# Kernel tuning notes

Measured on AMD Instinct MI355X. Metric: run time of the kernel, lower is better.

The kernel has to match this reference:

```python
import jax, jax.numpy as jnp
import numpy as np

N = 50000       # nodes
E = 800000      # edges
D_IN = 128      # input_dim
HID = 256       # hidden_dim
HEADS = 4
FH = HID // 4   # per-head out dim = 64
OUT = 8         # output_dim
NEG_SLOPE = 0.2 # GATConv leaky_relu slope


def setup_inputs() -> dict:
    key = jax.random.key(0)
    ks = jax.random.split(key, 16)
    def glorot(k, shape):
        fan_in, fan_out = shape[0], shape[-1]
        s = jnp.sqrt(6.0 / (fan_in + fan_out))
        return jax.random.uniform(k, shape, jnp.float32, -s, s)
    inp = {
        "x": jax.random.normal(ks[0], (N, D_IN), jnp.float32),
        "edge_index": jax.random.randint(ks[1], (2, E), 0, N, jnp.int64),
        # GCN layers
        "W1": glorot(ks[2], (D_IN, HID)), "b1": jnp.zeros((HID,), jnp.float32),
        "W2": glorot(ks[3], (HID, HID)), "b2": jnp.zeros((HID,), jnp.float32),
        "W3": glorot(ks[4], (HID, HID // 2)), "b3": jnp.zeros((HID // 2,), jnp.float32),
        # GAT layer: in = HID//2 = 128, out per head = FH, 4 heads concat -> HID
        "Wg": glorot(ks[5], (HID // 2, HEADS * FH)),
        "a_src": glorot(ks[6], (HEADS, FH)),
        "a_dst": glorot(ks[7], (HEADS, FH)),
        "bg": jnp.zeros((HEADS * FH,), jnp.float32),
        # classifier MLP: HID -> HID//2 -> HID//4 -> OUT
        "Wc1": glorot(ks[8], (HID, HID // 2)), "bc1": jnp.zeros((HID // 2,), jnp.float32),
        "Wc2": glorot(ks[9], (HID // 2, HID // 4)), "bc2": jnp.zeros((HID // 4,), jnp.float32),
        "Wc3": glorot(ks[10], (HID // 4, OUT)), "bc3": jnp.zeros((OUT,), jnp.float32),
    }
    return inp


def _with_self_loops(edge_index, n):
    loop = jnp.arange(n, dtype=edge_index.dtype)
    src = jnp.concatenate([edge_index[0], loop])
    dst = jnp.concatenate([edge_index[1], loop])
    return src, dst


def gcn_conv(x, W, b, src, dst, n):
    # PyG GCNConv: h = X W; out = D^{-1/2}(A+I)D^{-1/2} h + b (self loops in src/dst)
    h = x @ W
    deg = jax.ops.segment_sum(jnp.ones_like(dst, jnp.float32), dst, num_segments=n)
    dinv = jnp.where(deg > 0, jax.lax.rsqrt(deg), 0.0)
    norm = dinv[src] * dinv[dst]                      # [E+N]
    out = jax.ops.segment_sum(h[src] * norm[:, None], dst, num_segments=n)
    return out + b


def gat_conv(x, Wg, a_src, a_dst, bg, src, dst, n):
    # PyG GATConv (eval mode, no attn dropout), self loops included in src/dst
    h = (x @ Wg).reshape(n, HEADS, FH)                # [N,H,F]
    al_s = jnp.einsum('nhf,hf->nh', h, a_src)         # [N,H]
    al_d = jnp.einsum('nhf,hf->nh', h, a_dst)
    e = jax.nn.leaky_relu(al_s[src] + al_d[dst], NEG_SLOPE)  # [E+N,H]
    m = jax.ops.segment_max(e, dst, num_segments=n)   # per-dst stable softmax
    ex = jnp.exp(e - m[dst])
    den = jax.ops.segment_sum(ex, dst, num_segments=n)
    alpha = ex / den[dst]                             # [E+N,H]
    out = jax.ops.segment_sum(h[src] * alpha[:, :, None], dst, num_segments=n)
    return out.reshape(n, HEADS * FH) + bg


def reference(x, edge_index, W1, b1, W2, b2, W3, b3, Wg, a_src, a_dst, bg,
              Wc1, bc1, Wc2, bc2, Wc3, bc3):
    n = x.shape[0]
    src, dst = _with_self_loops(edge_index, n)
    h1 = jax.nn.relu(gcn_conv(x, W1, b1, src, dst, n))
    h2 = jax.nn.relu(gcn_conv(h1, W2, b2, src, dst, n)) + h1
    h3 = jax.nn.relu(gcn_conv(h2, W3, b3, src, dst, n))
    h_att = jax.nn.relu(gat_conv(h3, Wg, a_src, a_dst, bg, src, dst, n))
    h_pooled = jnp.mean(h_att, axis=0, keepdims=True)           # [1, HID]
    z = jax.nn.relu(h_pooled @ Wc1 + bc1)
    z = jax.nn.relu(z @ Wc2 + bc2)
    return z @ Wc3 + bc3                                        # [1, OUT]
```

## Files before the change

### kernel.cpp

```cpp
#include <hip/hip_runtime.h>
#include <hip/hip_bf16.h>

#define NNODES 50000
#define NEDGES 800000
#define EN 850000
#define SCAN_B 196

typedef __attribute__((ext_vector_type(8))) short bf16x8;
typedef __attribute__((ext_vector_type(4))) float f32x4;

__device__ __forceinline__ float bf2f(unsigned short u) {
    return __uint_as_float(((unsigned)u) << 16);
}
__device__ __forceinline__ float bflo(unsigned u) { return __uint_as_float(u << 16); }
__device__ __forceinline__ float bfhi(unsigned u) { return __uint_as_float(u & 0xffff0000u); }
__device__ __forceinline__ unsigned short f2bf(float x) {
    unsigned u = __float_as_uint(x);
    u += 0x7fffu + ((u >> 16) & 1u);
    return (unsigned short)(u >> 16);
}
__device__ __forceinline__ unsigned pack2bf(float a, float b) {
    return (unsigned)f2bf(a) | ((unsigned)f2bf(b) << 16);
}
__device__ __forceinline__ void acc8(float* acc, uint4 v, float wg) {
    acc[0] += bflo(v.x) * wg; acc[1] += bfhi(v.x) * wg;
    acc[2] += bflo(v.y) * wg; acc[3] += bfhi(v.y) * wg;
    acc[4] += bflo(v.z) * wg; acc[5] += bfhi(v.z) * wg;
    acc[6] += bflo(v.w) * wg; acc[7] += bfhi(v.w) * wg;
}

__global__ __launch_bounds__(256) void deg_kernel(const int* __restrict__ ei, float* __restrict__ deg) {
    int e = blockIdx.x * blockDim.x + threadIdx.x;
    if (e < NEDGES) atomicAdd(&deg[ei[NEDGES + e]], 1.0f);
}

__global__ __launch_bounds__(256) void scan_part1(const float* __restrict__ deg, int* __restrict__ row,
                                                  int* __restrict__ bsum, float* __restrict__ dinv) {
    __shared__ int sdata[256];
    int t = threadIdx.x;
    int idx = blockIdx.x * 256 + t;
    float dg = idx < NNODES ? deg[idx] : 0.f;
    if (idx < NNODES) dinv[idx] = rsqrtf(dg + 1.0f);
    int v = idx < NNODES ? (int)dg + 1 : 0;
    sdata[t] = v;
    __syncthreads();
    for (int off = 1; off < 256; off <<= 1) {
        int tmp = t >= off ? sdata[t - off] : 0;
        __syncthreads();
        sdata[t] += tmp;
        __syncthreads();
    }
    if (idx < NNODES) row[idx] = sdata[t] - v;
    if (t == 255) bsum[blockIdx.x] = sdata[255];
}

__global__ __launch_bounds__(256) void scan_part2(int* __restrict__ bsum, int* __restrict__ bofs,
                                                  int* __restrict__ row) {
    __shared__ int sdata[256];
    int t = threadIdx.x;
    int v = t < SCAN_B ? bsum[t] : 0;
    sdata[t] = v;
    __syncthreads();
    for (int off = 1; off < 256; off <<= 1) {
        int tmp = t >= off ? sdata[t - off] : 0;
        __syncthreads();
        sdata[t] += tmp;
        __syncthreads();
    }
    if (t < SCAN_B) bofs[t] = sdata[t] - v;
    if (t == 0) row[NNODES] = EN;
}

__global__ __launch_bounds__(256) void scan_part3(int* __restrict__ row, const int* __restrict__ bofs) {
    int idx = blockIdx.x * 256 + threadIdx.x;
    if (idx < NNODES) row[idx] += bofs[blockIdx.x];
}

__global__ __launch_bounds__(256) void scatter_kernel(const int* __restrict__ ei, const int* __restrict__ row,
                                                      int* __restrict__ cursor, const float* __restrict__ dinv,
                                                      uint2* __restrict__ csr) {
    int e = blockIdx.x * blockDim.x + threadIdx.x;
    if (e >= EN) return;
    int s, d;
    if (e < NEDGES) { s = ei[e]; d = ei[NEDGES + e]; } else { s = e - NEDGES; d = s; }
    int pos = row[d] + atomicAdd(&cursor[d], 1);
    csr[pos] = make_uint2((unsigned)s, __float_as_uint(dinv[s] * dinv[d]));
}

__global__ __launch_bounds__(256) void tobf16_kernel(const float* __restrict__ in, unsigned short* __restrict__ out,
                                                     int total8) {
    int i = blockIdx.x * 256 + threadIdx.x;
    if (i >= total8) return;
    float4 a = *(const float4*)&in[(size_t)i * 8];
    float4 b = *(const float4*)&in[(size_t)i * 8 + 4];
    uint4 o;
    o.x = pack2bf(a.x, a.y); o.y = pack2bf(a.z, a.w);
    o.z = pack2bf(b.x, b.y); o.w = pack2bf(b.z, b.w);
    *(uint4*)&out[(size_t)i * 8] = o;
}

__device__ __forceinline__ void split_bf(float x, unsigned short& h, unsigned short& l) {
    unsigned u = __float_as_uint(x);
    h = (unsigned short)(u >> 16);
    float r = x - __uint_as_float(u & 0xffff0000u);
    l = (unsigned short)(__float_as_uint(r) >> 16);
}

__device__ __forceinline__ void do_split(const float* W, unsigned short* Wh, unsigned short* Wl,
                                         int i, int K, int N) {
    int n = i / K, k = i - n * K;
    unsigned short h, l;
    split_bf(W[(size_t)k * N + n], h, l);
    Wh[i] = h; Wl[i] = l;
}

__global__ __launch_bounds__(256) void wsplit4_kernel(const float* __restrict__ W1, const float* __restrict__ W2,
                                                      const float* __restrict__ W3, const float* __restrict__ Wg,
                                                      unsigned short* __restrict__ W1th, unsigned short* __restrict__ W1tl,
                                                      unsigned short* __restrict__ W2th, unsigned short* __restrict__ W2tl,
                                                      unsigned short* __restrict__ W3th, unsigned short* __restrict__ W3tl,
                                                      unsigned short* __restrict__ Wgth, unsigned short* __restrict__ Wgtl) {
    int idx = blockIdx.x * 256 + threadIdx.x;
    if (idx < 32768)        do_split(W1, W1th, W1tl, idx, 128, 256);
    else if (idx < 98304)   do_split(W2, W2th, W2tl, idx - 32768, 256, 256);
    else if (idx < 131072)  do_split(W3, W3th, W3tl, idx - 98304, 256, 128);
    else if (idx < 163840)  do_split(Wg, Wgth, Wgtl, idx - 131072, 128, 256);
}

template<int MODE>
__global__ __launch_bounds__(256) void gemm_bf(const unsigned short* __restrict__ A,
                                               const unsigned short* __restrict__ Wth,
                                               const unsigned short* __restrict__ Wtl,
                                               const float* __restrict__ bias,
                                               unsigned short* __restrict__ C, int M, int K, int Nc) {
    __shared__ unsigned short As[128][40];
    __shared__ unsigned short Bh[128][40], Bl[128][40];
    int t = threadIdx.x;
    int row0 = blockIdx.x * 128, col0 = blockIdx.y * 128;
    int lane = t & 63, w = t >> 6;
    int mb = (w >> 1) * 64, nb = (w & 1) * 64;
    int lr = lane & 15, kg = (lane >> 4) * 8;

    f32x4 acc[4][4];
#pragma unroll
    for (int i = 0; i < 4; ++i)
#pragma unroll
        for (int j = 0; j < 4; ++j) acc[i][j] = (f32x4){0.f, 0.f, 0.f, 0.f};

    for (int k0 = 0; k0 < K; k0 += 32) {
#pragma unroll
        for (int it = 0; it < 2; ++it) {
            int q = it * 256 + t;
            int row = q >> 2, seg = (q & 3) * 8;
            int grow = row0 + row;
            uint4 v = make_uint4(0, 0, 0, 0);
            if (grow < M) v = *(const uint4*)&A[(size_t)grow * K + k0 + seg];
            *(uint4*)&As[row][seg] = v;
        }
#pragma unroll
        for (int it = 0; it < 2; ++it) {
            int o = it * 256 + t;
            int n = o >> 2, ko = (o & 3) * 8;
            size_t g = (size_t)(col0 + n) * K + k0 + ko;
            *(uint4*)&Bh[n][ko] = *(const uint4*)&Wth[g];
            *(uint4*)&Bl[n][ko] = *(const uint4*)&Wtl[g];
        }
        __syncthreads();

        bf16x8 a[4], bh[4], bl[4];
#pragma unroll
        for (int mf = 0; mf < 4; ++mf) a[mf] = *(const bf16x8*)&As[mb + mf * 16 + lr][kg];
#pragma unroll
        for (int nf = 0; nf < 4; ++nf) {
            bh[nf] = *(const bf16x8*)&Bh[nb + nf * 16 + lr][kg];
            bl[nf] = *(const bf16x8*)&Bl[nb + nf * 16 + lr][kg];
        }
#pragma unroll
        for (int mf = 0; mf < 4; ++mf)
#pragma unroll
            for (int nf = 0; nf < 4; ++nf) {
                acc[mf][nf] = __builtin_amdgcn_mfma_f32_16x16x32_bf16(a[mf], bh[nf], acc[mf][nf], 0, 0, 0);
                acc[mf][nf] = __builtin_amdgcn_mfma_f32_16x16x32_bf16(a[mf], bl[nf], acc[mf][nf], 0, 0, 0);
            }
        __syncthreads();
    }

#pragma unroll
    for (int nf = 0; nf < 4; ++nf) {
        int col = col0 + nb + nf * 16 + lr;
        float bv = (MODE == 1) ? bias[col] : 0.f;
#pragma unroll
        for (int mf = 0; mf < 4; ++mf) {
#pragma unroll
            for (int r = 0; r < 4; ++r) {
                int row = row0 + mb + mf * 16 + (lane >> 4) * 4 + r;
                if (row < M) {
                    float v = acc[mf][nf][r];
                    if (MODE == 1) v = fmaxf(v + bv, 0.f);
                    C[(size_t)row * Nc + col] = f2bf(v);
                }
            }
        }
    }
}

template<int NC, int MODE>
__global__ __launch_bounds__(256) void gcn_agg_bf(const unsigned short* __restrict__ h, const int* __restrict__ row,
                                                  const uint2* __restrict__ csr,
                                                  const float* __restrict__ b, const unsigned short* __restrict__ res,
                                                  unsigned short* __restrict__ out) {
    int wid = (int)((blockIdx.x * blockDim.x + threadIdx.x) >> 6);
    if (wid >= NNODES) return;
    int lane = threadIdx.x & 63;
    constexpr int LPE = NC / 8;
    constexpr int EPI = 64 / LPE;
    int sub = lane / LPE, li = lane % LPE;
    int col = li * 8;
    float acc[8];
#pragma unroll
    for (int i = 0; i < 8; ++i) acc[i] = 0.f;
    int j0 = row[wid], j1 = row[wid + 1];
    int j = j0 + sub;
    for (; j + EPI < j1; j += 2 * EPI) {
        uint2 c0 = csr[j], c1 = csr[j + EPI];
        uint4 v0 = *(const uint4*)&h[(size_t)c0.x * NC + col];
        uint4 v1 = *(const uint4*)&h[(size_t)c1.x * NC + col];
        acc8(acc, v0, __uint_as_float(c0.y));
        acc8(acc, v1, __uint_as_float(c1.y));
    }
    if (j < j1) {
        uint2 c0 = csr[j];
        uint4 v0 = *(const uint4*)&h[(size_t)c0.x * NC + col];
        acc8(acc, v0, __uint_as_float(c0.y));
    }
#pragma unroll
    for (int i = 0; i < 8; ++i) {
        acc[i] += __shfl_xor(acc[i], 32);
        if constexpr (EPI == 4) acc[i] += __shfl_xor(acc[i], 16);
    }
    if (lane < LPE) {
        if constexpr (MODE >= 1) {
#pragma unroll
            for (int i = 0; i < 8; ++i) acc[i] = fmaxf(acc[i] + b[col + i], 0.f);
        }
        if constexpr (MODE == 2) {
            uint4 rv = *(const uint4*)&res[(size_t)wid * NC + col];
            acc8(acc, rv, 1.0f);
        }
        uint4 o;
        o.x = pack2bf(acc[0], acc[1]); o.y = pack2bf(acc[2], acc[3]);
        o.z = pack2bf(acc[4], acc[5]); o.w = pack2bf(acc[6], acc[7]);
        *(uint4*)&out[(size_t)wid * NC + col] = o;
    }
}

__global__ __launch_bounds__(256) void att_logits(const unsigned short* __restrict__ hg,
                                                  const float* __restrict__ a_src, const float* __restrict__ a_dst,
                                                  float* __restrict__ als, float* __restrict__ ald) {
    int gid = blockIdx.x * blockDim.x + threadIdx.x;
    if (gid >= NNODES * 4) return;
    int n = gid >> 2, h = gid & 3;
    const unsigned short* hr = hg + (size_t)n * 256 + h * 64;
    const float* as_ = a_src + h * 64;
    const float* ad_ = a_dst + h * 64;
    float s1 = 0.f, s2 = 0.f;
#pragma unroll
    for (int f = 0; f < 64; f += 8) {
        uint4 v = *(const uint4*)&hr[f];
        float x0 = bflo(v.x), x1 = bfhi(v.x), x2 = bflo(v.y), x3 = bfhi(v.y);
        float x4 = bflo(v.z), x5 = bfhi(v.z), x6 = bflo(v.w), x7 = bfhi(v.w);
        s1 += x0 * as_[f] + x1 * as_[f + 1] + x2 * as_[f + 2] + x3 * as_[f + 3]
            + x4 * as_[f + 4] + x5 * as_[f + 5] + x6 * as_[f + 6] + x7 * as_[f + 7];
        s2 += x0 * ad_[f] + x1 * ad_[f + 1] + x2 * ad_[f + 2] + x3 * ad_[f + 3]
            + x4 * ad_[f + 4] + x5 * ad_[f + 5] + x6 * ad_[f + 6] + x7 * ad_[f + 7];
    }
    als[gid] = s1; ald[gid] = s2;
}

__device__ __forceinline__ float lrelu(float x) { return x < 0.f ? 0.2f * x : x; }

__global__ __launch_bounds__(256) void gat_csr(const unsigned short* __restrict__ hg, const int* __restrict__ row,
                                               const uint2* __restrict__ csr, const float* __restrict__ als,
                                               const float* __restrict__ ald, const float* __restrict__ bg,
                                               unsigned short* __restrict__ out) {
    int wid = (int)((blockIdx.x * blockDim.x + threadIdx.x) >> 6);
    if (wid >= NNODES) return;
    int lane = threadIdx.x & 63;
    int j0 = row[wid], j1 = row[wid + 1];
    int deg = j1 - j0;
    float4 ad = *(const float4*)&ald[wid * 4];

    float m0 = -1e30f, m1 = -1e30f, m2 = -1e30f, m3 = -1e30f;
    float d0 = 0.f, d1 = 0.f, d2 = 0.f, d3 = 0.f;
    if (deg <= 64) {
        float e0 = -1e30f, e1 = -1e30f, e2 = -1e30f, e3 = -1e30f;
        if (lane < deg) {
            int s = (int)csr[j0 + lane].x;
            float4 as4 = *(const float4*)&als[s * 4];
            e0 = lrelu(as4.x + ad.x); e1 = lrelu(as4.y + ad.y);
            e2 = lrelu(as4.z + ad.z); e3 = lrelu(as4.w + ad.w);
        }
        m0 = e0; m1 = e1; m2 = e2; m3 = e3;
#pragma unroll
        for (int off = 32; off >= 1; off >>= 1) {
            m0 = fmaxf(m0, __shfl_xor(m0, off));
            m1 = fmaxf(m1, __shfl_xor(m1, off));
            m2 = fmaxf(m2, __shfl_xor(m2, off));
            m3 = fmaxf(m3, __shfl_xor(m3, off));
        }
        d0 = __expf(e0 - m0); d1 = __expf(e1 - m1);
        d2 = __expf(e2 - m2); d3 = __expf(e3 - m3);
#pragma unroll
        for (int off = 32; off >= 1; off >>= 1) {
            d0 += __shfl_xor(d0, off);
            d1 += __shfl_xor(d1, off);
            d2 += __shfl_xor(d2, off);
            d3 += __shfl_xor(d3, off);
        }
    } else {
        for (int j = j0 + lane; j < j1; j += 64) {
            int s = (int)csr[j].x;
            float4 as4 = *(const float4*)&als[s * 4];
            m0 = fmaxf(m0, lrelu(as4.x + ad.x));
            m1 = fmaxf(m1, lrelu(as4.y + ad.y));
            m2 = fmaxf(m2, lrelu(as4.z + ad.z));
            m3 = fmaxf(m3, lrelu(as4.w + ad.w));
        }
#pragma unroll
        for (int off = 32; off >= 1; off >>= 1) {
            m0 = fmaxf(m0, __shfl_xor(m0, off));
            m1 = fmaxf(m1, __shfl_xor(m1, off));
            m2 = fmaxf(m2, __shfl_xor(m2, off));
            m3 = fmaxf(m3, __shfl_xor(m3, off));
        }
        for (int j = j0 + lane; j < j1; j += 64) {
            int s = (int)csr[j].x;
            float4 as4 = *(const float4*)&als[s * 4];
            d0 += __expf(lrelu(as4.x + ad.x) - m0);
            d1 += __expf(lrelu(as4.y + ad.y) - m1);
            d2 += __expf(lrelu(as4.z + ad.z) - m2);
            d3 += __expf(lrelu(as4.w + ad.w) - m3);
        }
#pragma unroll
        for (int off = 32; off >= 1; off >>= 1) {
            d0 += __shfl_xor(d0, off);
            d1 += __shfl_xor(d1, off);
            d2 += __shfl_xor(d2, off);
            d3 += __shfl_xor(d3, off);
        }
    }

    int sub = lane >> 5, li = lane & 31;
    int h = li >> 3;
    float mh   = h == 0 ? m0 : h == 1 ? m1 : h == 2 ? m2 : m3;
    float invh = 1.f / (h == 0 ? d0 : h == 1 ? d1 : h == 2 ? d2 : d3);
    float adh  = h == 0 ? ad.x : h == 1 ? ad.y : h == 2 ? ad.z : ad.w;
    int col = li * 8;
    float acc[8];
#pragma unroll
    for (int i = 0; i < 8; ++i) acc[i] = 0.f;
    int j = j0 + sub;
    for (; j + 2 < j1; j += 4) {
        uint2 c0 = csr[j], c1 = csr[j + 2];
        float a0 = __expf(lrelu(als[c0.x * 4 + h] + adh) - mh) * invh;
        float a1 = __expf(lrelu(als[c1.x * 4 + h] + adh) - mh) * invh;
        uint4 v0 = *(const uint4*)&hg[(size_t)c0.x * 256 + col];
        uint4 v1 = *(const uint4*)&hg[(size_t)c1.x * 256 + col];
        acc8(acc, v0, a0);
        acc8(acc, v1, a1);
    }
    if (j < j1) {
        uint2 c0 = csr[j];
        float a0 = __expf(lrelu(als[c0.x * 4 + h] + adh) - mh) * invh;
        uint4 v0 = *(const uint4*)&hg[(size_t)c0.x * 256 + col];
        acc8(acc, v0, a0);
    }
#pragma unroll
    for (int i = 0; i < 8; ++i) acc[i] += __shfl_xor(acc[i], 32);
    if (lane < 32) {
        uint4 o;
        o.x = pack2bf(fmaxf(acc[0] + bg[col], 0.f),     fmaxf(acc[1] + bg[col + 1], 0.f));
        o.y = pack2bf(fmaxf(acc[2] + bg[col + 2], 0.f), fmaxf(acc[3] + bg[col + 3], 0.f));
        o.z = pack2bf(fmaxf(acc[4] + bg[col + 4], 0.f), fmaxf(acc[5] + bg[col + 5], 0.f));
        o.w = pack2bf(fmaxf(acc[6] + bg[col + 6], 0.f), fmaxf(acc[7] + bg[col + 7], 0.f));
        *(uint4*)&out[(size_t)wid * 256 + col] = o;
    }
}

__global__ __launch_bounds__(256) void pool_kernel(const unsigned short* __restrict__ hatt, float* __restrict__ pooled) {
    int col = threadIdx.x;
    int r0 = blockIdx.x * 256;
    int r1 = r0 + 256 < NNODES ? r0 + 256 : NNODES;
    float s = 0.f;
    for (int r = r0; r < r1; ++r) s += bf2f(hatt[(size_t)r * 256 + col]);
    atomicAdd(&pooled[col], s);
}

__global__ __launch_bounds__(256) void mlp_kernel(const float* __restrict__ pooled,
                                                  const float* __restrict__ Wc1, const float* __restrict__ bc1,
                                                  const float* __restrict__ Wc2, const float* __restrict__ bc2,
                                                  const float* __restrict__ Wc3, const float* __restrict__ bc3,
                                                  float* __restrict__ out) {
    __shared__ float p[256], z1[128], z2[64];
    int t = threadIdx.x;
    p[t] = pooled[t] * (1.0f / NNODES);
    __syncthreads();
    if (t < 128) {
        float s = bc1[t];
        for (int k = 0; k < 256; ++k) s += p[k] * Wc1[k * 128 + t];
        z1[t] = fmaxf(s, 0.f);
    }
    __syncthreads();
    if (t < 64) {
        float s = bc2[t];
        for (int k = 0; k < 128; ++k) s += z1[k] * Wc2[k * 64 + t];
        z2[t] = fmaxf(s, 0.f);
    }
    __syncthreads();
    if (t < 8) {
        float s = bc3[t];
        for (int k = 0; k < 64; ++k) s += z2[k] * Wc3[k * 8 + t];
        out[t] = s;
    }
}

extern "C" void kernel_launch(void* const* d_in, const int* in_sizes, int n_in,
                              void* d_out, int out_size, void* d_ws, size_t ws_size,
                              hipStream_t stream) {
    const float* x   = (const float*)d_in[0];
    const int*   ei  = (const int*)d_in[1];
    const float* W1  = (const float*)d_in[2];  const float* b1  = (const float*)d_in[3];
    const float* W2  = (const float*)d_in[4];  const float* b2  = (const float*)d_in[5];
    const float* W3  = (const float*)d_in[6];  const float* b3  = (const float*)d_in[7];
    const float* Wg  = (const float*)d_in[8];
    const float* asr = (const float*)d_in[9];  const float* ads = (const float*)d_in[10];
    const float* bg  = (const float*)d_in[11];
    const float* Wc1 = (const float*)d_in[12]; const float* bc1 = (const float*)d_in[13];
    const float* Wc2 = (const float*)d_in[14]; const float* bc2 = (const float*)d_in[15];
    const float* Wc3 = (const float*)d_in[16]; const float* bc3 = (const float*)d_in[17];
    float* out = (float*)d_out;

    char* w = (char*)d_ws;
    float* deg    = (float*)w; w += (size_t)NNODES * 4;
    float* dinv   = (float*)w; w += (size_t)NNODES * 4;
    int*   rowp   = (int*)w;   w += 200016;
    int*   cursor = (int*)w;   w += (size_t)NNODES * 4;
    int*   bsum   = (int*)w;   w += 256 * 4;
    int*   bofs   = (int*)w;   w += 256 * 4;
    uint2* csr    = (uint2*)w; w += (size_t)EN * 8;
    float* als    = (float*)w; w += (size_t)NNODES * 4 * 4;
    float* ald    = (float*)w; w += (size_t)NNODES * 4 * 4;
    float* pooled = (float*)w; w += 256 * 4;
    unsigned short* W1th = (unsigned short*)w; w += 128 * 256 * 2;
    unsigned short* W1tl = (unsigned short*)w; w += 128 * 256 * 2;
    unsigned short* W2th = (unsigned short*)w; w += 256 * 256 * 2;
    unsigned short* W2tl = (unsigned short*)w; w += 256 * 256 * 2;
    unsigned short* W3th = (unsigned short*)w; w += 256 * 128 * 2;
    unsigned short* W3tl = (unsigned short*)w; w += 256 * 128 * 2;
    unsigned short* Wgth = (unsigned short*)w; w += 128 * 256 * 2;
    unsigned short* Wgtl = (unsigned short*)w; w += 128 * 256 * 2;
    unsigned short* U1 = (unsigned short*)w; w += (size_t)NNODES * 256 * 2;
    unsigned short* U2 = (unsigned short*)w; w += (size_t)NNODES * 256 * 2;
    unsigned short* U3 = (unsigned short*)w; w += (size_t)NNODES * 256 * 2;
    unsigned short* U4 = (unsigned short*)w; w += (size_t)NNODES * 256 * 2;

    hipMemsetAsync(deg, 0, (size_t)NNODES * 4, stream);
    hipMemsetAsync(cursor, 0, (size_t)NNODES * 4, stream);
    deg_kernel<<<(NEDGES + 255) / 256, 256, 0, stream>>>(ei, deg);
    scan_part1<<<SCAN_B, 256, 0, stream>>>(deg, rowp, bsum, dinv);
    scan_part2<<<1, 256, 0, stream>>>(bsum, bofs, rowp);
    scan_part3<<<SCAN_B, 256, 0, stream>>>(rowp, bofs);
    scatter_kernel<<<(EN + 255) / 256, 256, 0, stream>>>(ei, rowp, cursor, dinv, csr);

    wsplit4_kernel<<<640, 256, 0, stream>>>(W1, W2, W3, Wg, W1th, W1tl, W2th, W2tl, W3th, W3tl, Wgth, Wgtl);
    tobf16_kernel<<<(NNODES * 128 / 8 + 255) / 256, 256, 0, stream>>>(x, U1, NNODES * 128 / 8);

    dim3 gA((NNODES + 127) / 128, 2);
    dim3 gB((NNODES + 127) / 128, 1);
    int aggBlocks = (NNODES * 64 + 255) / 256;

    gcn_agg_bf<128, 0><<<aggBlocks, 256, 0, stream>>>(U1, rowp, csr, nullptr, nullptr, U2);
    gemm_bf<1><<<gA, 256, 0, stream>>>(U2, W1th, W1tl, b1, U3, NNODES, 128, 256);

    gemm_bf<0><<<gA, 256, 0, stream>>>(U3, W2th, W2tl, nullptr, U1, NNODES, 256, 256);
    gcn_agg_bf<256, 2><<<aggBlocks, 256, 0, stream>>>(U1, rowp, csr, b2, U3, U2);

    gemm_bf<0><<<gB, 256, 0, stream>>>(U2, W3th, W3tl, nullptr, U4, NNODES, 256, 128);
    gcn_agg_bf<128, 1><<<aggBlocks, 256, 0, stream>>>(U4, rowp, csr, b3, nullptr, U1);

    gemm_bf<0><<<gA, 256, 0, stream>>>(U1, Wgth, Wgtl, nullptr, U2, NNODES, 128, 256);
    att_logits<<<(NNODES * 4 + 255) / 256, 256, 0, stream>>>(U2, asr, ads, als, ald);
    gat_csr<<<aggBlocks, 256, 0, stream>>>(U2, rowp, csr, als, ald, bg, U3);

    hipMemsetAsync(pooled, 0, 256 * 4, stream);
    pool_kernel<<<(NNODES + 255) / 256, 256, 0, stream>>>(U3, pooled);
    mlp_kernel<<<1, 256, 0, stream>>>(pooled, Wc1, bc1, Wc2, bc2, Wc3, bc3, out);
}
```

Before: 550.0 us.

## Fuse prep kernels, unroll GCN aggregation, cache GAT softmax weights in LDS

Merges degree counting, the x-to-bf16 conversion and the weight split into one prep kernel sized exactly to 800000 threads (3125 blocks), removing two launches. The GCN aggregation loop is unrolled to four edges in flight for more memory-level parallelism. For nodes with degree up to 64, the GAT kernel computes normalized attention weights once per edge into shared memory and broadcasts source indices by shuffle, instead of re-reading csr/als and recomputing exp per lane in the gather loop. This trades extra LDS use and registers for fewer redundant loads and transcendentals.

Result: faster. 538.3 us (-2.1%).

```diff
diff --git a/kernel.cpp b/kernel.cpp
--- a/kernel.cpp
+++ b/kernel.cpp
@@ -29,9 +29,42 @@
     acc[6] += bflo(v.w) * wg; acc[7] += bfhi(v.w) * wg;
 }
 
-__global__ __launch_bounds__(256) void deg_kernel(const int* __restrict__ ei, float* __restrict__ deg) {
-    int e = blockIdx.x * blockDim.x + threadIdx.x;
-    if (e < NEDGES) atomicAdd(&deg[ei[NEDGES + e]], 1.0f);
+__device__ __forceinline__ void split_bf(float x, unsigned short& h, unsigned short& l) {
+    unsigned u = __float_as_uint(x);
+    h = (unsigned short)(u >> 16);
+    float r = x - __uint_as_float(u & 0xffff0000u);
+    l = (unsigned short)(__float_as_uint(r) >> 16);
+}
+__device__ __forceinline__ void do_split(const float* W, unsigned short* Wh, unsigned short* Wl,
+                                         int i, int K, int N) {
+    int n = i / K, k = i - n * K;
+    unsigned short h, l;
+    split_bf(W[(size_t)k * N + n], h, l);
+    Wh[i] = h; Wl[i] = l;
+}
+
+__global__ __launch_bounds__(256) void prep_kernel(const int* __restrict__ ei, float* __restrict__ deg,
+                                                   const float* __restrict__ x, unsigned short* __restrict__ xbf,
+                                                   const float* __restrict__ W1, const float* __restrict__ W2,
+                                                   const float* __restrict__ W3, const float* __restrict__ Wg,
+                                                   unsigned short* __restrict__ W1th, unsigned short* __restrict__ W1tl,
+                                                   unsigned short* __restrict__ W2th, unsigned short* __restrict__ W2tl,
+                                                   unsigned short* __restrict__ W3th, unsigned short* __restrict__ W3tl,
+                                                   unsigned short* __restrict__ Wgth, unsigned short* __restrict__ Wgtl) {
+    int idx = blockIdx.x * 256 + threadIdx.x;
+    atomicAdd(&deg[ei[NEDGES + idx]], 1.0f);
+    {
+        float4 a = *(const float4*)&x[(size_t)idx * 8];
+        float4 b = *(const float4*)&x[(size_t)idx * 8 + 4];
+        uint4 o;
+        o.x = pack2bf(a.x, a.y); o.y = pack2bf(a.z, a.w);
+        o.z = pack2bf(b.x, b.y); o.w = pack2bf(b.z, b.w);
+        *(uint4*)&xbf[(size_t)idx * 8] = o;
+    }
+    if (idx < 32768)        do_split(W1, W1th, W1tl, idx, 128, 256);
+    else if (idx < 98304)   do_split(W2, W2th, W2tl, idx - 32768, 256, 256);
+    else if (idx < 131072)  do_split(W3, W3th, W3tl, idx - 98304, 256, 128);
+    else if (idx < 163840)  do_split(Wg, Wgth, Wgtl, idx - 131072, 128, 256);
 }
 
 __global__ __launch_bounds__(256) void scan_part1(const float* __restrict__ deg, int* __restrict__ row,
@@ -87,46 +120,6 @@
     csr[pos] = make_uint2((unsigned)s, __float_as_uint(dinv[s] * dinv[d]));
 }
 
-__global__ __launch_bounds__(256) void tobf16_kernel(const float* __restrict__ in, unsigned short* __restrict__ out,
-                                                     int total8) {
-    int i = blockIdx.x * 256 + threadIdx.x;
-    if (i >= total8) return;
-    float4 a = *(const float4*)&in[(size_t)i * 8];
-    float4 b = *(const float4*)&in[(size_t)i * 8 + 4];
-    uint4 o;
-    o.x = pack2bf(a.x, a.y); o.y = pack2bf(a.z, a.w);
-    o.z = pack2bf(b.x, b.y); o.w = pack2bf(b.z, b.w);
-    *(uint4*)&out[(size_t)i * 8] = o;
-}
-
-__device__ __forceinline__ void split_bf(float x, unsigned short& h, unsigned short& l) {
-    unsigned u = __float_as_uint(x);
-    h = (unsigned short)(u >> 16);
-    float r = x - __uint_as_float(u & 0xffff0000u);
-    l = (unsigned short)(__float_as_uint(r) >> 16);
-}
-
-__device__ __forceinline__ void do_split(const float* W, unsigned short* Wh, unsigned short* Wl,
-                                         int i, int K, int N) {
-    int n = i / K, k = i - n * K;
-    unsigned short h, l;
-    split_bf(W[(size_t)k * N + n], h, l);
-    Wh[i] = h; Wl[i] = l;
-}
-
-__global__ __launch_bounds__(256) void wsplit4_kernel(const float* __restrict__ W1, const float* __restrict__ W2,
-                                                      const float* __restrict__ W3, const float* __restrict__ Wg,
-                                                      unsigned short* __restrict__ W1th, unsigned short* __restrict__ W1tl,
-                                                      unsigned short* __restrict__ W2th, unsigned short* __restrict__ W2tl,
-                                                      unsigned short* __restrict__ W3th, unsigned short* __restrict__ W3tl,
-                                                      unsigned short* __restrict__ Wgth, unsigned short* __restrict__ Wgtl) {
-    int idx = blockIdx.x * 256 + threadIdx.x;
-    if (idx < 32768)        do_split(W1, W1th, W1tl, idx, 128, 256);
-    else if (idx < 98304)   do_split(W2, W2th, W2tl, idx - 32768, 256, 256);
-    else if (idx < 131072)  do_split(W3, W3th, W3tl, idx - 98304, 256, 128);
-    else if (idx < 163840)  do_split(Wg, Wgth, Wgtl, idx - 131072, 128, 256);
-}
-
 template<int MODE>
 __global__ __launch_bounds__(256) void gemm_bf(const unsigned short* __restrict__ A,
                                                const unsigned short* __restrict__ Wth,
@@ -221,14 +214,18 @@
     for (int i = 0; i < 8; ++i) acc[i] = 0.f;
     int j0 = row[wid], j1 = row[wid + 1];
     int j = j0 + sub;
-    for (; j + EPI < j1; j += 2 * EPI) {
-        uint2 c0 = csr[j], c1 = csr[j + EPI];
+    for (; j + 3 * EPI < j1; j += 4 * EPI) {
+        uint2 c0 = csr[j], c1 = csr[j + EPI], c2 = csr[j + 2 * EPI], c3 = csr[j + 3 * EPI];
         uint4 v0 = *(const uint4*)&h[(size_t)c0.x * NC + col];
         uint4 v1 = *(const uint4*)&h[(size_t)c1.x * NC + col];
+        uint4 v2 = *(const uint4*)&h[(size_t)c2.x * NC + col];
+        uint4 v3 = *(const uint4*)&h[(size_t)c3.x * NC + col];
         acc8(acc, v0, __uint_as_float(c0.y));
         acc8(acc, v1, __uint_as_float(c1.y));
-    }
-    if (j < j1) {
+        acc8(acc, v2, __uint_as_float(c2.y));
+        acc8(acc, v3, __uint_as_float(c3.y));
+    }
+    for (; j < j1; j += EPI) {
         uint2 c0 = csr[j];
         uint4 v0 = *(const uint4*)&h[(size_t)c0.x * NC + col];
         acc8(acc, v0, __uint_as_float(c0.y));
@@ -283,24 +280,31 @@
                                                const uint2* __restrict__ csr, const float* __restrict__ als,
                                                const float* __restrict__ ald, const float* __restrict__ bg,
                                                unsigned short* __restrict__ out) {
+    __shared__ float alds[4][64][4];
     int wid = (int)((blockIdx.x * blockDim.x + threadIdx.x) >> 6);
     if (wid >= NNODES) return;
+    int wv = threadIdx.x >> 6;
     int lane = threadIdx.x & 63;
     int j0 = row[wid], j1 = row[wid + 1];
     int deg = j1 - j0;
     float4 ad = *(const float4*)&ald[wid * 4];
-
-    float m0 = -1e30f, m1 = -1e30f, m2 = -1e30f, m3 = -1e30f;
-    float d0 = 0.f, d1 = 0.f, d2 = 0.f, d3 = 0.f;
+    int sub = lane >> 5, li = lane & 31;
+    int h = li >> 3;
+    int col = li * 8;
+    float acc[8];
+#pragma unroll
+    for (int i = 0; i < 8; ++i) acc[i] = 0.f;
+
     if (deg <= 64) {
+        int sreg = 0;
         float e0 = -1e30f, e1 = -1e30f, e2 = -1e30f, e3 = -1e30f;
         if (lane < deg) {
-            int s = (int)csr[j0 + lane].x;
-            float4 as4 = *(const float4*)&als[s * 4];
+            sreg = (int)csr[j0 + lane].x;
+            float4 as4 = *(const float4*)&als[sreg * 4];
             e0 = lrelu(as4.x + ad.x); e1 = lrelu(as4.y + ad.y);
             e2 = lrelu(as4.z + ad.z); e3 = lrelu(as4.w + ad.w);
         }
-        m0 = e0; m1 = e1; m2 = e2; m3 = e3;
+        float m0 = e0, m1 = e1, m2 = e2, m3 = e3;
 #pragma unroll
         for (int off = 32; off >= 1; off >>= 1) {
             m0 = fmaxf(m0, __shfl_xor(m0, off));
@@ -308,8 +312,9 @@
             m2 = fmaxf(m2, __shfl_xor(m2, off));
             m3 = fmaxf(m3, __shfl_xor(m3, off));
         }
-        d0 = __expf(e0 - m0); d1 = __expf(e1 - m1);
-        d2 = __expf(e2 - m2); d3 = __expf(e3 - m3);
+        float x0 = __expf(e0 - m0), x1 = __expf(e1 - m1);
+        float x2 = __expf(e2 - m2), x3 = __expf(e3 - m3);
+        float d0 = x0, d1 = x1, d2 = x2, d3 = x3;
 #pragma unroll
         for (int off = 32; off >= 1; off >>= 1) {
             d0 += __shfl_xor(d0, off);
@@ -317,7 +322,30 @@
             d2 += __shfl_xor(d2, off);
             d3 += __shfl_xor(d3, off);
         }
+        float i0 = 1.f / d0, i1 = 1.f / d1, i2 = 1.f / d2, i3 = 1.f / d3;
+        *(float4*)&alds[wv][lane][0] = make_float4(x0 * i0, x1 * i1, x2 * i2, x3 * i3);
+        int k = sub;
+        for (; k + 6 < deg; k += 8) {
+            int s0 = __shfl(sreg, k),     s1 = __shfl(sreg, k + 2);
+            int s2 = __shfl(sreg, k + 4), s3 = __shfl(sreg, k + 6);
+            float a0 = alds[wv][k][h],     a1 = alds[wv][k + 2][h];
+            float a2 = alds[wv][k + 4][h], a3 = alds[wv][k + 6][h];
+            uint4 v0 = *(const uint4*)&hg[(size_t)s0 * 256 + col];
+            uint4 v1 = *(const uint4*)&hg[(size_t)s1 * 256 + col];
+            uint4 v2 = *(const uint4*)&hg[(size_t)s2 * 256 + col];
+            uint4 v3 = *(const uint4*)&hg[(size_t)s3 * 256 + col];
+            acc8(acc, v0, a0); acc8(acc, v1, a1);
+            acc8(acc, v2, a2); acc8(acc, v3, a3);
+        }
+        for (; k < deg; k += 2) {
+            int s0 = __shfl(sreg, k);
+            float a0 = alds[wv][k][h];
+            uint4 v0 = *(const uint4*)&hg[(size_t)s0 * 256 + col];
+            acc8(acc, v0, a0);
+        }
     } else {
+        float m0 = -1e30f, m1 = -1e30f, m2 = -1e30f, m3 = -1e30f;
+        float d0 = 0.f, d1 = 0.f, d2 = 0.f, d3 = 0.f;
         for (int j = j0 + lane; j < j1; j += 64) {
             int s = (int)csr[j].x;
             float4 as4 = *(const float4*)&als[s * 4];
@@ -348,33 +376,17 @@
             d2 += __shfl_xor(d2, off);
             d3 += __shfl_xor(d3, off);
         }
-    }
-
-    int sub = lane >> 5, li = lane & 31;
-    int h = li >> 3;
-    float mh   = h == 0 ? m0 : h == 1 ? m1 : h == 2 ? m2 : m3;
-    float invh = 1.f / (h == 0 ? d0 : h == 1 ? d1 : h == 2 ? d2 : d3);
-    float adh  = h == 0 ? ad.x : h == 1 ? ad.y : h == 2 ? ad.z : ad.w;
-    int col = li * 8;
-    float acc[8];
-#pragma unroll
-    for (int i = 0; i < 8; ++i) acc[i] = 0.f;
-    int j = j0 + sub;
-    for (; j + 2 < j1; j += 4) {
-        uint2 c0 = csr[j], c1 = csr[j + 2];
-        float a0 = __expf(lrelu(als[c0.x * 4 + h] + adh) - mh) * invh;
-        float a1 = __expf(lrelu(als[c1.x * 4 + h] + adh) - mh) * invh;
-        uint4 v0 = *(const uint4*)&hg[(size_t)c0.x * 256 + col];
-        uint4 v1 = *(const uint4*)&hg[(size_t)c1.x * 256 + col];
-        acc8(acc, v0, a0);
-        acc8(acc, v1, a1);
-    }
-    if (j < j1) {
-        uint2 c0 = csr[j];
-        float a0 = __expf(lrelu(als[c0.x * 4 + h] + adh) - mh) * invh;
-        uint4 v0 = *(const uint4*)&hg[(size_t)c0.x * 256 + col];
-        acc8(acc, v0, a0);
-    }
+        float mh   = h == 0 ? m0 : h == 1 ? m1 : h == 2 ? m2 : m3;
+        float invh = 1.f / (h == 0 ? d0 : h == 1 ? d1 : h == 2 ? d2 : d3);
+        float adh  = h == 0 ? ad.x : h == 1 ? ad.y : h == 2 ? ad.z : ad.w;
+        for (int j = j0 + sub; j < j1; j += 2) {
+            uint2 c0 = csr[j];
+            float a0 = __expf(lrelu(als[c0.x * 4 + h] + adh) - mh) * invh;
+            uint4 v0 = *(const uint4*)&hg[(size_t)c0.x * 256 + col];
+            acc8(acc, v0, a0);
+        }
+    }
+
 #pragma unroll
     for (int i = 0; i < 8; ++i) acc[i] += __shfl_xor(acc[i], 32);
     if (lane < 32) {
@@ -466,15 +478,13 @@
 
     hipMemsetAsync(deg, 0, (size_t)NNODES * 4, stream);
     hipMemsetAsync(cursor, 0, (size_t)NNODES * 4, stream);
-    deg_kernel<<<(NEDGES + 255) / 256, 256, 0, stream>>>(ei, deg);
+    prep_kernel<<<3125, 256, 0, stream>>>(ei, deg, x, U1, W1, W2, W3, Wg,
+                                          W1th, W1tl, W2th, W2tl, W3th, W3tl, Wgth, Wgtl);
     scan_part1<<<SCAN_B, 256, 0, stream>>>(deg, rowp, bsum, dinv);
     scan_part2<<<1, 256, 0, stream>>>(bsum, bofs, rowp);
     scan_part3<<<SCAN_B, 256, 0, stream>>>(rowp, bofs);
     scatter_kernel<<<(EN + 255) / 256, 256, 0, stream>>>(ei, rowp, cursor, dinv, csr);
 
-    wsplit4_kernel<<<640, 256, 0, stream>>>(W1, W2, W3, Wg, W1th, W1tl, W2th, W2tl, W3th, W3tl, Wgth, Wgtl);
-    tobf16_kernel<<<(NNODES * 128 / 8 + 255) / 256, 256, 0, stream>>>(x, U1, NNODES * 128 / 8);
-
     dim3 gA((NNODES + 127) / 128, 2);
     dim3 gB((NNODES + 127) / 128, 1);
     int aggBlocks = (NNODES * 64 + 255) / 256;
```
